# Kernel tuning notes

Hardware: AMD Instinct MI355X
Metric: run time of the kernel (lower is better)

Reference implementation:

```python
import jax, jax.numpy as jnp
import numpy as np

IN_FEATURES = 4096
OUT_FEATURES = 4096
R = 16

def setup_inputs() -> dict:
    key = jax.random.key(0)
    k1, k2 = jax.random.split(key)
    x = jax.random.normal(k1, (4, 2048, IN_FEATURES), dtype=jnp.float32)
    # Original init: B = zeros, A = randn. Use randn for B too so the output
    # is non-trivial for correctness testing (math is identical regardless).
    lora_matrix_B = jax.random.normal(k2, (OUT_FEATURES, R), dtype=jnp.float32) * 0.02
    lora_matrix_A = jax.random.normal(jax.random.fold_in(key, 1), (R, IN_FEATURES), dtype=jnp.float32)
    return {"x": x, "lora_matrix_B": lora_matrix_B, "lora_matrix_A": lora_matrix_A}

def reference(x, lora_matrix_B, lora_matrix_A):
    # lora_weights = B @ A  -> [out_features, in_features]
    lora_weights = jnp.matmul(lora_matrix_B, lora_matrix_A)
    # F.linear(x, W) = x @ W^T
    return jnp.einsum('bsi,oi->bso', x, lora_weights)
```

## Files before the change

### kernel.cpp

```cpp
#include <hip/hip_runtime.h>

#define K_DIM   4096
#define N_DIM   4096
#define M_ROWS  8192
#define KF      (K_DIM / 4)
#define NF      (N_DIM / 4)
#define KSPLIT  8
#define NTILES  (M_ROWS / 16)
#define TP_F4_STRIDE (M_ROWS * 16 / 4)
#define XAT_BLOCKS ((M_ROWS / 64) * KSPLIT)
#define TRB_BLOCKS 64

typedef __attribute__((ext_vector_type(8))) short short8v;
typedef __attribute__((ext_vector_type(4))) float f32x4;

static __device__ __forceinline__ short f2bf(float f) {
    const unsigned u = __builtin_bit_cast(unsigned, f);
    return (short)((u + 0x7FFFu + ((u >> 16) & 1u)) >> 16);
}

__global__ __launch_bounds__(256) void lora_xat(const float* __restrict__ x,
                                                const float* __restrict__ A,
                                                const float* __restrict__ B,
                                                float* __restrict__ Bt,
                                                float* __restrict__ tpart) {
    const int tid = threadIdx.x;

    if (blockIdx.x >= XAT_BLOCKS) {
        const int i4 = (blockIdx.x - XAT_BLOCKS) * 256 + tid;
        const int r  = i4 >> 10;
        const int c0 = (i4 & 1023) * 4;
        float4 v;
        v.x = B[(size_t)(c0 + 0) * 16 + r];
        v.y = B[(size_t)(c0 + 1) * 16 + r];
        v.z = B[(size_t)(c0 + 2) * 16 + r];
        v.w = B[(size_t)(c0 + 3) * 16 + r];
        ((float4*)Bt)[i4] = v;
        return;
    }

    const int wv   = tid >> 6;
    const int lane = tid & 63;
    const int rb   = blockIdx.x >> 3;
    const int h    = blockIdx.x & 7;
    const int row0 = rb * 64 + wv * 16;

    const int mrow = row0 + (lane & 15);
    const int acol = lane & 15;
    const int og   = (lane >> 4) * 2;

    const float4* x4 = (const float4*)x;
    const float4* A4 = (const float4*)A;
    const size_t xbase = (size_t)mrow * KF;
    const size_t abase = (size_t)acol * KF;

    f32x4 acc = {0.f, 0.f, 0.f, 0.f};

    #pragma unroll 4
    for (int it = 0; it < 16; ++it) {
        const int kf = h * 128 + it * 8 + og;
        const float4 xa = x4[xbase + kf];
        const float4 xb = x4[xbase + kf + 1];
        const float4 aa = A4[abase + kf];
        const float4 ab = A4[abase + kf + 1];

        short8v af, bf;
        af[0] = f2bf(xa.x); af[1] = f2bf(xa.y);
        af[2] = f2bf(xa.z); af[3] = f2bf(xa.w);
        af[4] = f2bf(xb.x); af[5] = f2bf(xb.y);
        af[6] = f2bf(xb.z); af[7] = f2bf(xb.w);
        bf[0] = f2bf(aa.x); bf[1] = f2bf(aa.y);
        bf[2] = f2bf(aa.z); bf[3] = f2bf(aa.w);
        bf[4] = f2bf(ab.x); bf[5] = f2bf(ab.y);
        bf[6] = f2bf(ab.z); bf[7] = f2bf(ab.w);

        acc = __builtin_amdgcn_mfma_f32_16x16x32_bf16(af, bf, acc, 0, 0, 0);
    }

    #pragma unroll
    for (int v = 0; v < 4; ++v) {
        const int orow = row0 + (lane >> 4) * 4 + v;
        tpart[((size_t)h * M_ROWS + orow) * 16 + (lane & 15)] = acc[v];
    }
}

__global__ __launch_bounds__(256) void lora_tb(const float* __restrict__ tpart,
                                               const float* __restrict__ Bt,
                                               float* __restrict__ out) {
    __shared__ float4 tp_s[4][64];
    __shared__ float4 t_s4[64];

    const int tid = threadIdx.x;
    const int rb  = blockIdx.x >> 2;
    const int cb  = blockIdx.x & 3;
    const int c4  = cb * 256 + tid;

    const float4* Bt4 = (const float4*)Bt;
    float4 bv[16];
    #pragma unroll
    for (int r = 0; r < 16; ++r)
        bv[r] = Bt4[r * NF + c4];

    {
        const int f  = tid & 63;
        const int hp = tid >> 6;
        const float4* p4 = (const float4*)tpart;
        float4 a = p4[(size_t)(2 * hp) * TP_F4_STRIDE + rb * 64 + f];
        const float4 b = p4[(size_t)(2 * hp + 1) * TP_F4_STRIDE + rb * 64 + f];
        a.x += b.x; a.y += b.y; a.z += b.z; a.w += b.w;
        tp_s[hp][f] = a;
    }
    __syncthreads();
    if (tid < 64) {
        float4 s = tp_s[0][tid];
        #pragma unroll
        for (int hp = 1; hp < 4; ++hp) {
            const float4 q = tp_s[hp][tid];
            s.x += q.x; s.y += q.y; s.z += q.z; s.w += q.w;
        }
        t_s4[tid] = s;
    }
    __syncthreads();

    float4* out4 = (float4*)out;

    #pragma unroll
    for (int row = 0; row < 16; ++row) {
        float4 tq[4];
        #pragma unroll
        for (int q = 0; q < 4; ++q)
            tq[q] = t_s4[row * 4 + q];
        float4 o = {0.f, 0.f, 0.f, 0.f};
        #pragma unroll
        for (int r = 0; r < 16; ++r) {
            const float4 tv4 = tq[r >> 2];
            const float tv = ((r & 3) == 0) ? tv4.x :
                             ((r & 3) == 1) ? tv4.y :
                             ((r & 3) == 2) ? tv4.z : tv4.w;
            o.x = fmaf(tv, bv[r].x, o.x);
            o.y = fmaf(tv, bv[r].y, o.y);
            o.z = fmaf(tv, bv[r].z, o.z);
            o.w = fmaf(tv, bv[r].w, o.w);
        }
        out4[(size_t)(rb * 16 + row) * NF + c4] = o;
    }
}

extern "C" void kernel_launch(void* const* d_in, const int* in_sizes, int n_in,
                              void* d_out, int out_size, void* d_ws, size_t ws_size,
                              hipStream_t stream) {
    const float* x = (const float*)d_in[0];
    const float* B = (const float*)d_in[1];
    const float* A = (const float*)d_in[2];
    float* out = (float*)d_out;

    float* Bt    = (float*)d_ws;
    float* tpart = Bt + 16 * N_DIM;

    lora_xat<<<XAT_BLOCKS + TRB_BLOCKS, 256, 0, stream>>>(x, A, B, Bt, tpart);
    lora_tb<<<NTILES * (N_DIM / 1024), 256, 0, stream>>>(tpart, Bt, out);
}
```

Before: 62.81 us.

## Fuse x·Aᵀ and t·Bᵀ stages into one kernel per 16-row tile

Replaces the split-K x·Aᵀ kernel plus separate t·B kernel with a single kernel per 16-row tile. Four waves each cover a quarter of K, reduce their partials in shared memory, and then write all 4096 output columns. This removes the global tpart round trip and the separate reduction launch. The trade-off is only 512 blocks, each doing longer serial work, and the B transpose stays in a small separate prep kernel.

```diff
diff --git a/kernel.cpp b/kernel.cpp
--- a/kernel.cpp
+++ b/kernel.cpp
@@ -5,11 +5,6 @@
 #define M_ROWS  8192
 #define KF      (K_DIM / 4)
 #define NF      (N_DIM / 4)
-#define KSPLIT  8
-#define NTILES  (M_ROWS / 16)
-#define TP_F4_STRIDE (M_ROWS * 16 / 4)
-#define XAT_BLOCKS ((M_ROWS / 64) * KSPLIT)
-#define TRB_BLOCKS 64
 
 typedef __attribute__((ext_vector_type(8))) short short8v;
 typedef __attribute__((ext_vector_type(4))) float f32x4;
@@ -19,31 +14,30 @@
     return (short)((u + 0x7FFFu + ((u >> 16) & 1u)) >> 16);
 }
 
-__global__ __launch_bounds__(256) void lora_xat(const float* __restrict__ x,
-                                                const float* __restrict__ A,
-                                                const float* __restrict__ B,
-                                                float* __restrict__ Bt,
-                                                float* __restrict__ tpart) {
-    const int tid = threadIdx.x;
+__global__ __launch_bounds__(256) void lora_prep(const float* __restrict__ B,
+                                                 float* __restrict__ Bt) {
+    const int i4 = blockIdx.x * 256 + threadIdx.x;
+    const int r  = i4 >> 10;
+    const int c0 = (i4 & 1023) * 4;
+    float4 v;
+    v.x = B[(size_t)(c0 + 0) * 16 + r];
+    v.y = B[(size_t)(c0 + 1) * 16 + r];
+    v.z = B[(size_t)(c0 + 2) * 16 + r];
+    v.w = B[(size_t)(c0 + 3) * 16 + r];
+    ((float4*)Bt)[i4] = v;
+}
 
-    if (blockIdx.x >= XAT_BLOCKS) {
-        const int i4 = (blockIdx.x - XAT_BLOCKS) * 256 + tid;
-        const int r  = i4 >> 10;
-        const int c0 = (i4 & 1023) * 4;
-        float4 v;
-        v.x = B[(size_t)(c0 + 0) * 16 + r];
-        v.y = B[(size_t)(c0 + 1) * 16 + r];
-        v.z = B[(size_t)(c0 + 2) * 16 + r];
-        v.w = B[(size_t)(c0 + 3) * 16 + r];
-        ((float4*)Bt)[i4] = v;
-        return;
-    }
+__global__ __launch_bounds__(256) void lora_fused(const float* __restrict__ x,
+                                                  const float* __restrict__ A,
+                                                  const float* __restrict__ Bt,
+                                                  float* __restrict__ out) {
+    __shared__ float part[4][256];
+    __shared__ float t_s[256];
 
+    const int tid  = threadIdx.x;
     const int wv   = tid >> 6;
     const int lane = tid & 63;
-    const int rb   = blockIdx.x >> 3;
-    const int h    = blockIdx.x & 7;
-    const int row0 = rb * 64 + wv * 16;
+    const int row0 = blockIdx.x * 16;
 
     const int mrow = row0 + (lane & 15);
     const int acol = lane & 15;
@@ -53,12 +47,13 @@
     const float4* A4 = (const float4*)A;
     const size_t xbase = (size_t)mrow * KF;
     const size_t abase = (size_t)acol * KF;
+    const int kq = wv * 256;
 
     f32x4 acc = {0.f, 0.f, 0.f, 0.f};
 
     #pragma unroll 4
-    for (int it = 0; it < 16; ++it) {
-        const int kf = h * 128 + it * 8 + og;
+    for (int it = 0; it < 32; ++it) {
+        const int kf = kq + it * 8 + og;
         const float4 xa = x4[xbase + kf];
         const float4 xb = x4[xbase + kf + 1];
         const float4 aa = A4[abase + kf];
@@ -78,71 +73,44 @@
     }
 
     #pragma unroll
-    for (int v = 0; v < 4; ++v) {
-        const int orow = row0 + (lane >> 4) * 4 + v;
-        tpart[((size_t)h * M_ROWS + orow) * 16 + (lane & 15)] = acc[v];
-    }
-}
+    for (int v = 0; v < 4; ++v)
+        part[wv][((lane >> 4) * 4 + v) * 16 + (lane & 15)] = acc[v];
+    __syncthreads();
 
-__global__ __launch_bounds__(256) void lora_tb(const float* __restrict__ tpart,
-                                               const float* __restrict__ Bt,
-                                               float* __restrict__ out) {
-    __shared__ float4 tp_s[4][64];
-    __shared__ float4 t_s4[64];
-
-    const int tid = threadIdx.x;
-    const int rb  = blockIdx.x >> 2;
-    const int cb  = blockIdx.x & 3;
-    const int c4  = cb * 256 + tid;
+    t_s[tid] = ((part[0][tid] + part[1][tid]) +
+                (part[2][tid] + part[3][tid]));
+    __syncthreads();
 
     const float4* Bt4 = (const float4*)Bt;
-    float4 bv[16];
-    #pragma unroll
-    for (int r = 0; r < 16; ++r)
-        bv[r] = Bt4[r * NF + c4];
-
-    {
-        const int f  = tid & 63;
-        const int hp = tid >> 6;
-        const float4* p4 = (const float4*)tpart;
-        float4 a = p4[(size_t)(2 * hp) * TP_F4_STRIDE + rb * 64 + f];
-        const float4 b = p4[(size_t)(2 * hp + 1) * TP_F4_STRIDE + rb * 64 + f];
-        a.x += b.x; a.y += b.y; a.z += b.z; a.w += b.w;
-        tp_s[hp][f] = a;
-    }
-    __syncthreads();
-    if (tid < 64) {
-        float4 s = tp_s[0][tid];
-        #pragma unroll
-        for (int hp = 1; hp < 4; ++hp) {
-            const float4 q = tp_s[hp][tid];
-            s.x += q.x; s.y += q.y; s.z += q.z; s.w += q.w;
-        }
-        t_s4[tid] = s;
-    }
-    __syncthreads();
-
+    const float4* ts4 = (const float4*)t_s;
     float4* out4 = (float4*)out;
 
-    #pragma unroll
-    for (int row = 0; row < 16; ++row) {
-        float4 tq[4];
+    for (int ch = 0; ch < 4; ++ch) {
+        const int c4 = ch * 256 + tid;
+        float4 bv[16];
         #pragma unroll
-        for (int q = 0; q < 4; ++q)
-            tq[q] = t_s4[row * 4 + q];
-        float4 o = {0.f, 0.f, 0.f, 0.f};
+        for (int r = 0; r < 16; ++r)
+            bv[r] = Bt4[r * NF + c4];
         #pragma unroll
-        for (int r = 0; r < 16; ++r) {
-            const float4 tv4 = tq[r >> 2];
-            const float tv = ((r & 3) == 0) ? tv4.x :
-                             ((r & 3) == 1) ? tv4.y :
-                             ((r & 3) == 2) ? tv4.z : tv4.w;
-            o.x = fmaf(tv, bv[r].x, o.x);
-            o.y = fmaf(tv, bv[r].y, o.y);
-            o.z = fmaf(tv, bv[r].z, o.z);
-            o.w = fmaf(tv, bv[r].w, o.w);
+        for (int row = 0; row < 16; ++row) {
+            float4 tq[4];
+            #pragma unroll
+            for (int q = 0; q < 4; ++q)
+                tq[q] = ts4[row * 4 + q];
+            float4 o = {0.f, 0.f, 0.f, 0.f};
+            #pragma unroll
+            for (int r = 0; r < 16; ++r) {
+                const float4 tv4 = tq[r >> 2];
+                const float tv = ((r & 3) == 0) ? tv4.x :
+                                 ((r & 3) == 1) ? tv4.y :
+                                 ((r & 3) == 2) ? tv4.z : tv4.w;
+                o.x = fmaf(tv, bv[r].x, o.x);
+                o.y = fmaf(tv, bv[r].y, o.y);
+                o.z = fmaf(tv, bv[r].z, o.z);
+                o.w = fmaf(tv, bv[r].w, o.w);
+            }
+            out4[(size_t)(row0 + row) * NF + c4] = o;
         }
-        out4[(size_t)(rb * 16 + row) * NF + c4] = o;
     }
 }
 
@@ -154,9 +122,8 @@
     const float* A = (const float*)d_in[2];
     float* out = (float*)d_out;
 
-    float* Bt    = (float*)d_ws;
-    float* tpart = Bt + 16 * N_DIM;
+    float* Bt = (float*)d_ws;
 
-    lora_xat<<<XAT_BLOCKS + TRB_BLOCKS, 256, 0, stream>>>(x, A, B, Bt, tpart);
-    lora_tb<<<NTILES * (N_DIM / 1024), 256, 0, stream>>>(tpart, Bt, out);
+    lora_prep<<<64, 256, 0, stream>>>(B, Bt);
+    lora_fused<<<M_ROWS / 16, 256, 0, stream>>>(x, A, Bt, out);
 }
```

After: 148.8 us. 137% more time.
